# Optimization experiments

Measured on AMD Instinct MI355X. Metric: run time of the kernel, lower is better.

Reference implementation:

```python
import jax, jax.numpy as jnp
import numpy as np

N = 4_000_000   # number of (parent, child) edges
N_RELS = 20
P = 3            # n_polarities
Z_EPS = 0.01
COS_EPS = 0.01
SCALE_FACTOR = 42.0


def setup_inputs() -> dict:
    key = jax.random.key(0)
    k1, k2, k3, k4, k5, k6, k7 = jax.random.split(key, 7)
    child_probs = jax.random.uniform(k1, (N, P), dtype=jnp.float32)
    prnt_probs = jax.random.uniform(k2, (N, P), dtype=jnp.float32)
    child_probs = child_probs * (jax.random.uniform(k3, (N, 1)) > 0.1).astype(jnp.float32)
    prnt_probs = prnt_probs * (jax.random.uniform(k4, (N, 1)) > 0.1).astype(jnp.float32)
    rels = jax.random.randint(k5, (N,), 0, N_RELS)
    eps_M = jax.random.normal(k6, (N, P, P), dtype=jnp.float32)
    beta = jax.random.beta(k7, 15.0, 15.0, (N,), dtype=jnp.float32)  # Beta(beta_p, beta_q), all 15.0
    # learned/fixed params per __init__
    MU = np.eye(P, dtype=np.float32)
    MU[1, :] = [-0.25, 0.5, -0.25]
    rel_mu = jnp.asarray(np.tile(MU, (N_RELS, 1)).reshape(N_RELS, P, P))
    rel_sigma = jnp.ones((N_RELS, P, P), dtype=jnp.float32)
    return {"prnt_probs": prnt_probs, "child_probs": child_probs, "rel_mu": rel_mu,
            "rel_sigma": rel_sigma, "eps_M": eps_M, "beta": beta, "rels": rels}


def _safe_norm(x):
    sq = jnp.sum(x * x, axis=-1)
    return jnp.where(sq == 0.0, 0.0, jnp.sqrt(jnp.where(sq == 0.0, 1.0, sq)))


def _scale(prnt, child):
    # z = max(eps, p + c); normalize; entropy; cosine similarity; scale = 42 * cos / H(z)
    z = jnp.maximum(Z_EPS, prnt + child)
    z = z / jnp.sum(z, axis=-1, keepdims=True)
    entropy = -jnp.sum(z * jnp.log(z), axis=-1)
    cos = jnp.sum(prnt * child, axis=-1)
    norm = _safe_norm(prnt) * _safe_norm(child)
    norm = jnp.where(norm == 0.0, 1.0, norm)
    cos = jnp.maximum(COS_EPS, cos / norm)
    return SCALE_FACTOR * cos / entropy


def reference(prnt_probs, child_probs, rel_mu, rel_sigma, eps_M, beta, rels):
    # mask-based equivalent of the nonzero()-gather version (static shapes for jit)
    child_mask = jnp.sum(child_probs, axis=-1) != 0.0          # rows with nonzero child probs
    # M ~ Normal(mu[rels], sigma[rels]) reparameterized
    M = rel_mu[rels] + rel_sigma[rels] * eps_M                  # [N, P, P]
    cp = jax.nn.softmax(jnp.einsum('nij,nj->ni', M, child_probs), axis=-1)  # [N, P]
    prnt_sum = jnp.sum(prnt_probs, axis=-1)
    copy_mask = child_mask & (prnt_sum == 0.0)                  # child copied to parent
    alpha_mask = child_mask & (prnt_sum != 0.0)                 # blended update
    s = _scale(prnt_probs, cp)                                  # [N]
    alpha = ((1.0 - beta)[:, None] * prnt_probs + beta[:, None] * cp) * s[:, None]
    child_probs2copy = jnp.where(copy_mask[:, None], cp, 0.0)
    alpha = jnp.where(alpha_mask[:, None], alpha, 0.0)
    return copy_mask, child_probs2copy, alpha_mask, alpha
```

## Files before the change

kernel.cpp:

```cpp
#include <hip/hip_runtime.h>

#define BLOCK 256
#define ROWS  256
#define PCF4  (ROWS * 3 / 4)
#define EPSF4 (ROWS * 9 / 4)

typedef const __attribute__((address_space(1))) void* gas1_t;
typedef __attribute__((address_space(3)))       void* las3_t;

__device__ __forceinline__ void ld_lds16(const float4* g, float4* l) {
    __builtin_amdgcn_global_load_lds((gas1_t)(const void*)g, (las3_t)(void*)l, 16, 0, 0);
}

__global__ __launch_bounds__(BLOCK, 8) void alpha_kernel(
    const float4* __restrict__ prnt4,
    const float4* __restrict__ child4,
    const float*  __restrict__ rel_mu,
    const float*  __restrict__ rel_sigma,
    const float4* __restrict__ eps4,
    const float*  __restrict__ beta,
    const int*    __restrict__ rels,
    float*  __restrict__ out0,
    float4* __restrict__ out1,
    float*  __restrict__ out2,
    float4* __restrict__ out3,
    int n_rows, int nmu)
{
    __shared__ float4 s_p[PCF4];
    __shared__ float4 s_c[PCF4];
    __shared__ float4 s_e[EPSF4];
    __shared__ float  smu[192];
    __shared__ float  ssg[192];

    const int  tid       = threadIdx.x;
    const int  lane      = tid & 63;
    const int  wv        = tid >> 6;
    const int  b         = blockIdx.x;
    const long rows_base = (long)b * ROWS;
    const int  rows_here = min(ROWS, (int)(n_rows - rows_base));
    const bool full      = (rows_here == ROWS);

    const float4* gp = prnt4  + (size_t)b * PCF4;
    const float4* gc = child4 + (size_t)b * PCF4;
    const float4* ge = eps4   + (size_t)b * EPSF4;

    float rmu = 0.0f, rsg = 0.0f;
    const bool has_mu = (tid < nmu);
    if (has_mu) { rmu = rel_mu[tid]; rsg = rel_sigma[tid]; }

    const bool active = (tid < rows_here);
    float bt = 0.0f;
    int   rq = 0;
    if (active) {
        bt = beta[rows_base + tid];
        rq = rels[rows_base + tid];
    }

    if (full) {
        for (int c = wv; c < PCF4 / 64; c += 4) {
            ld_lds16(gp + (c << 6) + lane, s_p + (c << 6));
            ld_lds16(gc + (c << 6) + lane, s_c + (c << 6));
        }
        for (int c = wv; c < EPSF4 / 64; c += 4) {
            ld_lds16(ge + (c << 6) + lane, s_e + (c << 6));
        }
    } else {
        const int pcf4_here  = rows_here * 3 / 4;
        const int epsf4_here = rows_here * 9 / 4;
        const int pc_chunks  = pcf4_here >> 6;
        const int eps_chunks = epsf4_here >> 6;
        for (int c = wv; c < pc_chunks; c += 4) {
            ld_lds16(gp + (c << 6) + lane, s_p + (c << 6));
            ld_lds16(gc + (c << 6) + lane, s_c + (c << 6));
        }
        for (int c = wv; c < eps_chunks; c += 4) {
            ld_lds16(ge + (c << 6) + lane, s_e + (c << 6));
        }
        for (int i = (pc_chunks << 6) + tid; i < pcf4_here; i += BLOCK) {
            s_p[i] = gp[i];
            s_c[i] = gc[i];
        }
        for (int i = (eps_chunks << 6) + tid; i < epsf4_here; i += BLOCK) {
            s_e[i] = ge[i];
        }
    }

    if (has_mu) { smu[tid] = rmu; ssg[tid] = rsg; }
    __syncthreads();

    float o1[3], o3[3];
    float m0 = 0.0f, m2 = 0.0f;

    if (active) {
        const float* pf = (const float*)s_p;
        const float* cf = (const float*)s_c;
        const float* ef = (const float*)s_e;

        float p[3], c[3], e[9];
        #pragma unroll
        for (int k = 0; k < 3; ++k) p[k] = pf[3 * tid + k];
        #pragma unroll
        for (int k = 0; k < 3; ++k) c[k] = cf[3 * tid + k];
        #pragma unroll
        for (int k = 0; k < 9; ++k) e[k] = ef[9 * tid + k];

        const float* mu = &smu[9 * rq];
        const float* sg = &ssg[9 * rq];

        float l[3];
        #pragma unroll
        for (int i = 0; i < 3; ++i) {
            float acc = 0.0f;
            #pragma unroll
            for (int j = 0; j < 3; ++j) {
                float m = fmaf(sg[3 * i + j], e[3 * i + j], mu[3 * i + j]);
                acc = fmaf(m, c[j], acc);
            }
            l[i] = acc;
        }
        float mx = fmaxf(l[0], fmaxf(l[1], l[2]));
        float e0 = __expf(l[0] - mx), e1 = __expf(l[1] - mx), e2 = __expf(l[2] - mx);
        float einv = 1.0f / (e0 + e1 + e2);
        float cp0 = e0 * einv, cp1 = e1 * einv, cp2 = e2 * einv;

        float csum = c[0] + c[1] + c[2];
        float psum = p[0] + p[1] + p[2];
        bool cmask = (csum != 0.0f);
        bool copy  = cmask && (psum == 0.0f);
        bool amask = cmask && (psum != 0.0f);

        float z0 = fmaxf(0.01f, p[0] + cp0);
        float z1 = fmaxf(0.01f, p[1] + cp1);
        float z2 = fmaxf(0.01f, p[2] + cp2);
        float zinv = 1.0f / (z0 + z1 + z2);
        z0 *= zinv; z1 *= zinv; z2 *= zinv;
        float ent = -(z0 * __logf(z0) + z1 * __logf(z1) + z2 * __logf(z2));
        float cosv = p[0] * cp0 + p[1] * cp1 + p[2] * cp2;
        float np2 = p[0] * p[0] + p[1] * p[1] + p[2] * p[2];
        float nc2 = cp0 * cp0 + cp1 * cp1 + cp2 * cp2;
        float npn = (np2 == 0.0f) ? 0.0f : sqrtf(np2);
        float ncn = (nc2 == 0.0f) ? 0.0f : sqrtf(nc2);
        float nrm = npn * ncn;
        nrm = (nrm == 0.0f) ? 1.0f : nrm;
        cosv = fmaxf(0.01f, cosv / nrm);
        float s = 42.0f * cosv / ent;

        float bb = bt, ob = 1.0f - bb;
        float a0 = fmaf(ob, p[0], bb * cp0) * s;
        float a1 = fmaf(ob, p[1], bb * cp1) * s;
        float a2 = fmaf(ob, p[2], bb * cp2) * s;

        m0 = copy  ? 1.0f : 0.0f;
        m2 = amask ? 1.0f : 0.0f;
        o1[0] = copy ? cp0 : 0.0f;
        o1[1] = copy ? cp1 : 0.0f;
        o1[2] = copy ? cp2 : 0.0f;
        o3[0] = amask ? a0 : 0.0f;
        o3[1] = amask ? a1 : 0.0f;
        o3[2] = amask ? a2 : 0.0f;
    }

    __syncthreads();

    if (active) {
        float* of1 = (float*)s_p;
        float* of3 = (float*)s_c;
        #pragma unroll
        for (int k = 0; k < 3; ++k) of1[3 * tid + k] = o1[k];
        #pragma unroll
        for (int k = 0; k < 3; ++k) of3[3 * tid + k] = o3[k];
        out0[rows_base + tid] = m0;
        out2[rows_base + tid] = m2;
    }
    __syncthreads();

    float4* g1 = out1 + (size_t)b * PCF4;
    float4* g3 = out3 + (size_t)b * PCF4;
    const int pcf4_here = rows_here * 3 / 4;
    for (int i = tid; i < pcf4_here; i += BLOCK) {
        g1[i] = s_p[i];
        g3[i] = s_c[i];
    }
}

extern "C" void kernel_launch(void* const* d_in, const int* in_sizes, int n_in,
                              void* d_out, int out_size, void* d_ws, size_t ws_size,
                              hipStream_t stream)
{
    const float* prnt      = (const float*)d_in[0];
    const float* child     = (const float*)d_in[1];
    const float* rel_mu    = (const float*)d_in[2];
    const float* rel_sigma = (const float*)d_in[3];
    const float* eps       = (const float*)d_in[4];
    const float* beta      = (const float*)d_in[5];
    const int*   rels      = (const int*)d_in[6];

    const int N   = in_sizes[5];
    const int nmu = in_sizes[2];

    float* out  = (float*)d_out;
    float* out0 = out;
    float* out1 = out + (size_t)N;
    float* out2 = out + (size_t)4 * N;
    float* out3 = out + (size_t)5 * N;

    int blocks = (N + ROWS - 1) / ROWS;
    alpha_kernel<<<blocks, BLOCK, 0, stream>>>(
        (const float4*)prnt, (const float4*)child, rel_mu, rel_sigma,
        (const float4*)eps, beta, rels,
        out0, (float4*)out1, out2, (float4*)out3,
        N, nmu);
}
```

Baseline: 329.7 us.

## Process four rows per thread with direct float4 global loads instead of LDS staging

Drops the LDS staging through global_load_lds. Each thread now handles four consecutive rows, which lets prnt, child, eps, beta, rels and every output be moved with aligned float4/int4 vector accesses straight to and from registers. This removes the shared-memory round trips and two of the block barriers. In exchange, per-thread accesses are strided (48 to 144 bytes per thread), so coalescing within a wavefront is worse, register pressure is higher, and there are a quarter as many threads to hide memory latency.

```diff
diff --git a/kernel.cpp b/kernel.cpp
--- a/kernel.cpp
+++ b/kernel.cpp
@@ -1,185 +1,155 @@
 #include <hip/hip_runtime.h>
 
 #define BLOCK 256
-#define ROWS  256
-#define PCF4  (ROWS * 3 / 4)
-#define EPSF4 (ROWS * 9 / 4)
+#define RPT   4
+#define RPB   (BLOCK * RPT)
 
-typedef const __attribute__((address_space(1))) void* gas1_t;
-typedef __attribute__((address_space(3)))       void* las3_t;
+__device__ __forceinline__ void row_compute(
+    const float* p, const float* c, const float* e,
+    float bb, int rq,
+    const float* smu, const float* ssg,
+    float* o1, float* o3, float& m0v, float& m2v)
+{
+    const float* mu = &smu[9 * rq];
+    const float* sg = &ssg[9 * rq];
 
-__device__ __forceinline__ void ld_lds16(const float4* g, float4* l) {
-    __builtin_amdgcn_global_load_lds((gas1_t)(const void*)g, (las3_t)(void*)l, 16, 0, 0);
+    float l[3];
+    #pragma unroll
+    for (int i = 0; i < 3; ++i) {
+        float acc = 0.0f;
+        #pragma unroll
+        for (int j = 0; j < 3; ++j) {
+            float m = fmaf(sg[3 * i + j], e[3 * i + j], mu[3 * i + j]);
+            acc = fmaf(m, c[j], acc);
+        }
+        l[i] = acc;
+    }
+    float mx = fmaxf(l[0], fmaxf(l[1], l[2]));
+    float e0 = __expf(l[0] - mx), e1 = __expf(l[1] - mx), e2 = __expf(l[2] - mx);
+    float einv = 1.0f / (e0 + e1 + e2);
+    float cp0 = e0 * einv, cp1 = e1 * einv, cp2 = e2 * einv;
+
+    float csum = c[0] + c[1] + c[2];
+    float psum = p[0] + p[1] + p[2];
+    bool cmask = (csum != 0.0f);
+    bool copy  = cmask && (psum == 0.0f);
+    bool amask = cmask && (psum != 0.0f);
+
+    float z0 = fmaxf(0.01f, p[0] + cp0);
+    float z1 = fmaxf(0.01f, p[1] + cp1);
+    float z2 = fmaxf(0.01f, p[2] + cp2);
+    float zinv = 1.0f / (z0 + z1 + z2);
+    z0 *= zinv; z1 *= zinv; z2 *= zinv;
+    float ent = -(z0 * __logf(z0) + z1 * __logf(z1) + z2 * __logf(z2));
+    float cosv = p[0] * cp0 + p[1] * cp1 + p[2] * cp2;
+    float np2 = p[0] * p[0] + p[1] * p[1] + p[2] * p[2];
+    float nc2 = cp0 * cp0 + cp1 * cp1 + cp2 * cp2;
+    float npn = (np2 == 0.0f) ? 0.0f : sqrtf(np2);
+    float ncn = (nc2 == 0.0f) ? 0.0f : sqrtf(nc2);
+    float nrm = npn * ncn;
+    nrm = (nrm == 0.0f) ? 1.0f : nrm;
+    cosv = fmaxf(0.01f, cosv / nrm);
+    float s = 42.0f * cosv / ent;
+
+    float ob = 1.0f - bb;
+    float a0 = fmaf(ob, p[0], bb * cp0) * s;
+    float a1 = fmaf(ob, p[1], bb * cp1) * s;
+    float a2 = fmaf(ob, p[2], bb * cp2) * s;
+
+    m0v = copy  ? 1.0f : 0.0f;
+    m2v = amask ? 1.0f : 0.0f;
+    o1[0] = copy ? cp0 : 0.0f;
+    o1[1] = copy ? cp1 : 0.0f;
+    o1[2] = copy ? cp2 : 0.0f;
+    o3[0] = amask ? a0 : 0.0f;
+    o3[1] = amask ? a1 : 0.0f;
+    o3[2] = amask ? a2 : 0.0f;
 }
 
-__global__ __launch_bounds__(BLOCK, 8) void alpha_kernel(
-    const float4* __restrict__ prnt4,
-    const float4* __restrict__ child4,
-    const float*  __restrict__ rel_mu,
-    const float*  __restrict__ rel_sigma,
-    const float4* __restrict__ eps4,
-    const float*  __restrict__ beta,
-    const int*    __restrict__ rels,
-    float*  __restrict__ out0,
-    float4* __restrict__ out1,
-    float*  __restrict__ out2,
-    float4* __restrict__ out3,
+__global__ __launch_bounds__(BLOCK, 2) void alpha_kernel(
+    const float* __restrict__ prnt,
+    const float* __restrict__ child,
+    const float* __restrict__ rel_mu,
+    const float* __restrict__ rel_sigma,
+    const float* __restrict__ eps,
+    const float* __restrict__ beta,
+    const int*  __restrict__ rels,
+    float* __restrict__ out0,
+    float* __restrict__ out1,
+    float* __restrict__ out2,
+    float* __restrict__ out3,
     int n_rows, int nmu)
 {
-    __shared__ float4 s_p[PCF4];
-    __shared__ float4 s_c[PCF4];
-    __shared__ float4 s_e[EPSF4];
-    __shared__ float  smu[192];
-    __shared__ float  ssg[192];
+    __shared__ float smu[192];
+    __shared__ float ssg[192];
 
-    const int  tid       = threadIdx.x;
-    const int  lane      = tid & 63;
-    const int  wv        = tid >> 6;
-    const int  b         = blockIdx.x;
-    const long rows_base = (long)b * ROWS;
-    const int  rows_here = min(ROWS, (int)(n_rows - rows_base));
-    const bool full      = (rows_here == ROWS);
-
-    const float4* gp = prnt4  + (size_t)b * PCF4;
-    const float4* gc = child4 + (size_t)b * PCF4;
-    const float4* ge = eps4   + (size_t)b * EPSF4;
-
-    float rmu = 0.0f, rsg = 0.0f;
-    const bool has_mu = (tid < nmu);
-    if (has_mu) { rmu = rel_mu[tid]; rsg = rel_sigma[tid]; }
-
-    const bool active = (tid < rows_here);
-    float bt = 0.0f;
-    int   rq = 0;
-    if (active) {
-        bt = beta[rows_base + tid];
-        rq = rels[rows_base + tid];
-    }
-
-    if (full) {
-        for (int c = wv; c < PCF4 / 64; c += 4) {
-            ld_lds16(gp + (c << 6) + lane, s_p + (c << 6));
-            ld_lds16(gc + (c << 6) + lane, s_c + (c << 6));
-        }
-        for (int c = wv; c < EPSF4 / 64; c += 4) {
-            ld_lds16(ge + (c << 6) + lane, s_e + (c << 6));
-        }
-    } else {
-        const int pcf4_here  = rows_here * 3 / 4;
-        const int epsf4_here = rows_here * 9 / 4;
-        const int pc_chunks  = pcf4_here >> 6;
-        const int eps_chunks = epsf4_here >> 6;
-        for (int c = wv; c < pc_chunks; c += 4) {
-            ld_lds16(gp + (c << 6) + lane, s_p + (c << 6));
-            ld_lds16(gc + (c << 6) + lane, s_c + (c << 6));
-        }
-        for (int c = wv; c < eps_chunks; c += 4) {
-            ld_lds16(ge + (c << 6) + lane, s_e + (c << 6));
-        }
-        for (int i = (pc_chunks << 6) + tid; i < pcf4_here; i += BLOCK) {
-            s_p[i] = gp[i];
-            s_c[i] = gc[i];
-        }
-        for (int i = (eps_chunks << 6) + tid; i < epsf4_here; i += BLOCK) {
-            s_e[i] = ge[i];
-        }
-    }
-
-    if (has_mu) { smu[tid] = rmu; ssg[tid] = rsg; }
+    const int tid = threadIdx.x;
+    if (tid < nmu) { smu[tid] = rel_mu[tid]; ssg[tid] = rel_sigma[tid]; }
     __syncthreads();
 
-    float o1[3], o3[3];
-    float m0 = 0.0f, m2 = 0.0f;
+    const long T  = (long)blockIdx.x * BLOCK + tid;
+    const long r0 = T * RPT;
+    if (r0 >= n_rows) return;
 
-    if (active) {
-        const float* pf = (const float*)s_p;
-        const float* cf = (const float*)s_c;
-        const float* ef = (const float*)s_e;
+    if (r0 + RPT <= n_rows) {
+        const float4* p4 = (const float4*)prnt;
+        const float4* c4 = (const float4*)child;
+        const float4* e4 = (const float4*)eps;
+        const float4* b4 = (const float4*)beta;
+        const int4*   r4 = (const int4*)rels;
 
-        float p[3], c[3], e[9];
+        float4 P[3], C[3], E[9];
         #pragma unroll
-        for (int k = 0; k < 3; ++k) p[k] = pf[3 * tid + k];
+        for (int k = 0; k < 3; ++k) P[k] = p4[3 * T + k];
         #pragma unroll
-        for (int k = 0; k < 3; ++k) c[k] = cf[3 * tid + k];
+        for (int k = 0; k < 3; ++k) C[k] = c4[3 * T + k];
         #pragma unroll
-        for (int k = 0; k < 9; ++k) e[k] = ef[9 * tid + k];
+        for (int k = 0; k < 9; ++k) E[k] = e4[9 * T + k];
+        float4 bt = b4[T];
+        int4   rl = r4[T];
 
-        const float* mu = &smu[9 * rq];
-        const float* sg = &ssg[9 * rq];
+        const float* Pf = (const float*)P;
+        const float* Cf = (const float*)C;
+        const float* Ef = (const float*)E;
+        float bq[RPT] = {bt.x, bt.y, bt.z, bt.w};
+        int   rq[RPT] = {rl.x, rl.y, rl.z, rl.w};
 
-        float l[3];
+        float o1[12], o3[12], m0[RPT], m2[RPT];
         #pragma unroll
-        for (int i = 0; i < 3; ++i) {
-            float acc = 0.0f;
+        for (int r = 0; r < RPT; ++r) {
+            row_compute(Pf + 3 * r, Cf + 3 * r, Ef + 9 * r,
+                        bq[r], rq[r], smu, ssg,
+                        o1 + 3 * r, o3 + 3 * r, m0[r], m2[r]);
+        }
+
+        ((float4*)out0)[T] = make_float4(m0[0], m0[1], m0[2], m0[3]);
+        ((float4*)out2)[T] = make_float4(m2[0], m2[1], m2[2], m2[3]);
+        float4* o1g = (float4*)out1;
+        float4* o3g = (float4*)out3;
+        const float4* o1l = (const float4*)o1;
+        const float4* o3l = (const float4*)o3;
+        #pragma unroll
+        for (int k = 0; k < 3; ++k) o1g[3 * T + k] = o1l[k];
+        #pragma unroll
+        for (int k = 0; k < 3; ++k) o3g[3 * T + k] = o3l[k];
+    } else {
+        for (long r = r0; r < n_rows; ++r) {
+            float p[3], c[3], e[9];
             #pragma unroll
-            for (int j = 0; j < 3; ++j) {
-                float m = fmaf(sg[3 * i + j], e[3 * i + j], mu[3 * i + j]);
-                acc = fmaf(m, c[j], acc);
-            }
-            l[i] = acc;
+            for (int k = 0; k < 3; ++k) p[k] = prnt[3 * r + k];
+            #pragma unroll
+            for (int k = 0; k < 3; ++k) c[k] = child[3 * r + k];
+            #pragma unroll
+            for (int k = 0; k < 9; ++k) e[k] = eps[9 * r + k];
+            float o1s[3], o3s[3], m0s, m2s;
+            row_compute(p, c, e, beta[r], rels[r], smu, ssg, o1s, o3s, m0s, m2s);
+            out0[r] = m0s;
+            out2[r] = m2s;
+            #pragma unroll
+            for (int k = 0; k < 3; ++k) out1[3 * r + k] = o1s[k];
+            #pragma unroll
+            for (int k = 0; k < 3; ++k) out3[3 * r + k] = o3s[k];
         }
-        float mx = fmaxf(l[0], fmaxf(l[1], l[2]));
-        float e0 = __expf(l[0] - mx), e1 = __expf(l[1] - mx), e2 = __expf(l[2] - mx);
-        float einv = 1.0f / (e0 + e1 + e2);
-        float cp0 = e0 * einv, cp1 = e1 * einv, cp2 = e2 * einv;
-
-        float csum = c[0] + c[1] + c[2];
-        float psum = p[0] + p[1] + p[2];
-        bool cmask = (csum != 0.0f);
-        bool copy  = cmask && (psum == 0.0f);
-        bool amask = cmask && (psum != 0.0f);
-
-        float z0 = fmaxf(0.01f, p[0] + cp0);
-        float z1 = fmaxf(0.01f, p[1] + cp1);
-        float z2 = fmaxf(0.01f, p[2] + cp2);
-        float zinv = 1.0f / (z0 + z1 + z2);
-        z0 *= zinv; z1 *= zinv; z2 *= zinv;
-        float ent = -(z0 * __logf(z0) + z1 * __logf(z1) + z2 * __logf(z2));
-        float cosv = p[0] * cp0 + p[1] * cp1 + p[2] * cp2;
-        float np2 = p[0] * p[0] + p[1] * p[1] + p[2] * p[2];
-        float nc2 = cp0 * cp0 + cp1 * cp1 + cp2 * cp2;
-        float npn = (np2 == 0.0f) ? 0.0f : sqrtf(np2);
-        float ncn = (nc2 == 0.0f) ? 0.0f : sqrtf(nc2);
-        float nrm = npn * ncn;
-        nrm = (nrm == 0.0f) ? 1.0f : nrm;
-        cosv = fmaxf(0.01f, cosv / nrm);
-        float s = 42.0f * cosv / ent;
-
-        float bb = bt, ob = 1.0f - bb;
-        float a0 = fmaf(ob, p[0], bb * cp0) * s;
-        float a1 = fmaf(ob, p[1], bb * cp1) * s;
-        float a2 = fmaf(ob, p[2], bb * cp2) * s;
-
-        m0 = copy  ? 1.0f : 0.0f;
-        m2 = amask ? 1.0f : 0.0f;
-        o1[0] = copy ? cp0 : 0.0f;
-        o1[1] = copy ? cp1 : 0.0f;
-        o1[2] = copy ? cp2 : 0.0f;
-        o3[0] = amask ? a0 : 0.0f;
-        o3[1] = amask ? a1 : 0.0f;
-        o3[2] = amask ? a2 : 0.0f;
-    }
-
-    __syncthreads();
-
-    if (active) {
-        float* of1 = (float*)s_p;
-        float* of3 = (float*)s_c;
-        #pragma unroll
-        for (int k = 0; k < 3; ++k) of1[3 * tid + k] = o1[k];
-        #pragma unroll
-        for (int k = 0; k < 3; ++k) of3[3 * tid + k] = o3[k];
-        out0[rows_base + tid] = m0;
-        out2[rows_base + tid] = m2;
-    }
-    __syncthreads();
-
-    float4* g1 = out1 + (size_t)b * PCF4;
-    float4* g3 = out3 + (size_t)b * PCF4;
-    const int pcf4_here = rows_here * 3 / 4;
-    for (int i = tid; i < pcf4_here; i += BLOCK) {
-        g1[i] = s_p[i];
-        g3[i] = s_c[i];
     }
 }
 
@@ -204,10 +174,8 @@
     float* out2 = out + (size_t)4 * N;
     float* out3 = out + (size_t)5 * N;
 
-    int blocks = (N + ROWS - 1) / ROWS;
+    int blocks = (N + RPB - 1) / RPB;
     alpha_kernel<<<blocks, BLOCK, 0, stream>>>(
-        (const float4*)prnt, (const float4*)child, rel_mu, rel_sigma,
-        (const float4*)eps, beta, rels,
-        out0, (float4*)out1, out2, (float4*)out3,
-        N, nmu);
+        prnt, child, rel_mu, rel_sigma, eps, beta, rels,
+        out0, out1, out2, out3, N, nmu);
 }
```

Result: slower. 355.5 us (+7.8%).
